# Optimization experiments

Measured on AMD Instinct MI355X. Metric: run time of the kernel, lower is better.

The kernel has to match this reference:

```python
import jax, jax.numpy as jnp
import numpy as np
from jax import lax

B, TIN, N, M, O, LM, TDEC = 64, 128, 256, 1024, 512, 2048, 64
LN_EPS = 1e-5


def setup_inputs() -> dict:
    key = jax.random.key(0)
    ks = jax.random.split(key, 32)
    s = 0.02
    p = lambda k, shape: (jax.random.normal(k, shape, jnp.float32) * s)
    z = lambda n: jnp.zeros((n,), jnp.float32)
    return {
        "X": jax.random.normal(ks[0], (B, TIN, N), jnp.float32),
        "Y0": jax.random.uniform(ks[1], (B, 1, O), jnp.float32),
        # encoder GRU, 2 layers (PyTorch layout: W_ih [3m,in], W_hh [3m,m])
        "enc_Wih0": p(ks[2], (3 * M, N)), "enc_Whh0": p(ks[3], (3 * M, M)),
        "enc_bih0": z(3 * M), "enc_bhh0": z(3 * M),
        "enc_Wih1": p(ks[4], (3 * M, M)), "enc_Whh1": p(ks[5], (3 * M, M)),
        "enc_bih1": z(3 * M), "enc_bhh1": z(3 * M),
        # decoder GRU, 2 layers (layer0 input dim = O)
        "dec_Wih0": p(ks[6], (3 * M, O)), "dec_Whh0": p(ks[7], (3 * M, M)),
        "dec_bih0": z(3 * M), "dec_bhh0": z(3 * M),
        "dec_Wih1": p(ks[8], (3 * M, M)), "dec_Whh1": p(ks[9], (3 * M, M)),
        "dec_bih1": z(3 * M), "dec_bhh1": z(3 * M),
        # decoder head
        "fc1_w": p(ks[10], (LM, M)), "fc1_b": z(LM),
        "ln_g": jnp.ones((LM,), jnp.float32), "ln_b": z(LM),
        "fc2_w": p(ks[11], (O, LM)), "fc2_b": z(O),
    }


def _gru_step(h, x, Wih, Whh, bih, bhh):
    # PyTorch GRU cell: gates ordered (r, z, n)
    gi = x @ Wih.T + bih          # [B, 3m]
    gh = h @ Whh.T + bhh          # [B, 3m]
    i_r, i_z, i_n = jnp.split(gi, 3, axis=-1)
    h_r, h_z, h_n = jnp.split(gh, 3, axis=-1)
    r = jax.nn.sigmoid(i_r + h_r)
    zg = jax.nn.sigmoid(i_z + h_z)
    n = jnp.tanh(i_n + r * h_n)
    return (1.0 - zg) * n + zg * h


def reference(X, Y0,
              enc_Wih0, enc_Whh0, enc_bih0, enc_bhh0,
              enc_Wih1, enc_Whh1, enc_bih1, enc_bhh1,
              dec_Wih0, dec_Whh0, dec_bih0, dec_bhh0,
              dec_Wih1, dec_Whh1, dec_bih1, dec_bhh1,
              fc1_w, fc1_b, ln_g, ln_b, fc2_w, fc2_b):
    batch = X.shape[0]
    # ---- encoder: 2-layer GRU over time ----
    seq = jnp.swapaxes(X, 0, 1)  # [T, B, n]
    enc_layers = [(enc_Wih0, enc_Whh0, enc_bih0, enc_bhh0),
                  (enc_Wih1, enc_Whh1, enc_bih1, enc_bhh1)]
    h_final = []
    for (Wih, Whh, bih, bhh) in enc_layers:
        def f(h, x, Wih=Wih, Whh=Whh, bih=bih, bhh=bhh):
            hn = _gru_step(h, x, Wih, Whh, bih, bhh)
            return hn, hn
        hT, seq = lax.scan(f, jnp.zeros((batch, M), X.dtype), seq)
        h_final.append(hT)

    dec0 = (dec_Wih0, dec_Whh0, dec_bih0, dec_bhh0)
    dec1 = (dec_Wih1, dec_Whh1, dec_bih1, dec_bhh1)
    y_init = Y0[:, 0, :]  # [B, o]

    def step(carry, _):
        h0, h1, y = carry
        h0n = _gru_step(h0, y, *dec0)
        h1n = _gru_step(h1, h0n, *dec1)
        z = h1n @ fc1_w.T + fc1_b                      # [B, l_m]
        mu = jnp.mean(z, axis=-1, keepdims=True)
        var = jnp.var(z, axis=-1, keepdims=True)
        z = (z - mu) * lax.rsqrt(var + LN_EPS) * ln_g + ln_b
        z = jax.nn.gelu(z, approximate=False)
        out = z @ fc2_w.T + fc2_b                      # [B, o]
        yn = jax.nn.softmax(out, axis=-1)
        return (h0n, h1n, yn), out

    _, outs = lax.scan(step, (h_final[0], h_final[1], y_init), None, length=TDEC)
    return jnp.swapaxes(outs, 0, 1)  # [B, TDEC, o]
```

## Files before the change

### kernel.cpp

```cpp
#include <hip/hip_runtime.h>
#include <math.h>

#define B 64
#define TIN 128
#define N_IN 256
#define M 1024
#define O_DIM 512
#define LM 2048
#define TDEC 64
#define M3 3072
#define CH 8

typedef short bf16x8 __attribute__((ext_vector_type(8)));
typedef float floatx4 __attribute__((ext_vector_type(4)));

__device__ __forceinline__ unsigned short f2bf(float f) {
    unsigned int u = __float_as_uint(f);
    u += 0x7FFFu + ((u >> 16) & 1u);
    return (unsigned short)(u >> 16);
}
__device__ __forceinline__ float sigm(float x) { return 1.f / (1.f + expf(-x)); }

__global__ __launch_bounds__(256) void cast_bf(const float* __restrict__ in,
                                               short* __restrict__ out, int n) {
    int i = blockIdx.x * 256 + threadIdx.x;
    if (i < n) out[i] = (short)f2bf(in[i]);
}

__global__ __launch_bounds__(256) void transpose_X_bf(const float* __restrict__ X,
                                                      short* __restrict__ Xt) {
    int idx = blockIdx.x * 256 + threadIdx.x;
    int n = idx & (N_IN - 1);
    int b = (idx >> 8) & (B - 1);
    int t = idx >> 14;
    Xt[idx] = (short)f2bf(X[(b * TIN + t) * N_IN + n]);
}

__global__ __launch_bounds__(256) void mfma_gemm_bias(
    const short* __restrict__ A, int lda,
    const short* __restrict__ W, int ldw,
    const float* __restrict__ bias,
    float* __restrict__ C, int ldc, int K) {
    int wave = threadIdx.x >> 6;
    int lane = threadIdx.x & 63;
    int r0 = blockIdx.y * 64 + wave * 16;
    int c0 = blockIdx.x * 16;
    int lrow = lane & 15;
    int ko8 = (lane >> 4) * 8;
    const short* ap = A + (size_t)(r0 + lrow) * lda + ko8;
    const short* wp = W + (size_t)(c0 + lrow) * ldw + ko8;
    floatx4 acc = {0.f, 0.f, 0.f, 0.f};
    #pragma unroll 4
    for (int k = 0; k < K; k += 32) {
        bf16x8 a = *(const bf16x8*)(ap + k);
        bf16x8 b = *(const bf16x8*)(wp + k);
        acc = __builtin_amdgcn_mfma_f32_16x16x32_bf16(a, b, acc, 0, 0, 0);
    }
    int col = c0 + lrow;
    float bv = bias[col];
    int rbase = r0 + (lane >> 4) * 4;
    #pragma unroll
    for (int i = 0; i < 4; i++)
        C[(size_t)(rbase + i) * ldc + col] = acc[i] + bv;
}

__global__ __launch_bounds__(256) void mfma_gemm_bias_ks(
    const short* __restrict__ A, int lda,
    const short* __restrict__ W, int ldw,
    const float* __restrict__ bias,
    float* __restrict__ C, int ldc, int K) {
    __shared__ float lds[4][64][4];
    int wave = threadIdx.x >> 6;
    int lane = threadIdx.x & 63;
    int r0 = blockIdx.y * 16;
    int c0 = blockIdx.x * 16;
    int Kq = K >> 2;
    int lrow = lane & 15;
    int ko8 = (lane >> 4) * 8;
    const short* ap = A + (size_t)(r0 + lrow) * lda + wave * Kq + ko8;
    const short* wp = W + (size_t)(c0 + lrow) * ldw + wave * Kq + ko8;
    floatx4 acc = {0.f, 0.f, 0.f, 0.f};
    #pragma unroll 4
    for (int k = 0; k < Kq; k += 32) {
        bf16x8 a = *(const bf16x8*)(ap + k);
        bf16x8 b = *(const bf16x8*)(wp + k);
        acc = __builtin_amdgcn_mfma_f32_16x16x32_bf16(a, b, acc, 0, 0, 0);
    }
    #pragma unroll
    for (int i = 0; i < 4; i++) lds[wave][lane][i] = acc[i];
    __syncthreads();
    int row = threadIdx.x >> 4, col = threadIdx.x & 15;
    int sl = (row >> 2) * 16 + col, rg = row & 3;
    float s = lds[0][sl][rg] + lds[1][sl][rg] + lds[2][sl][rg] + lds[3][sl][rg];
    C[(size_t)(r0 + row) * ldc + (c0 + col)] = s + bias[c0 + col];
}

__global__ __launch_bounds__(256) void gru_step_enc(
    const short* __restrict__ h_in_bf, const short* __restrict__ Whh,
    const float* __restrict__ gi, const float* __restrict__ bhh,
    float* __restrict__ h_f, short* __restrict__ h_out_bf,
    short* __restrict__ seq_out_bf) {
    __shared__ float lr[4][64][4], lz[4][64][4], lnn[4][64][4];
    int wave = threadIdx.x >> 6;
    int lane = threadIdx.x & 63;
    int m0 = blockIdx.x * 16;
    int r0 = blockIdx.y * 16;
    int lrow = lane & 15;
    int ko8 = (lane >> 4) * 8;
    const int Kq = M >> 2;
    const short* ap = h_in_bf + (size_t)(r0 + lrow) * M + wave * Kq + ko8;
    const short* wr = Whh + (size_t)(m0 + lrow) * M + wave * Kq + ko8;
    const short* wz = wr + (size_t)M * M;
    const short* wn = wr + (size_t)2 * M * M;
    floatx4 ar = {0.f, 0.f, 0.f, 0.f};
    floatx4 az = {0.f, 0.f, 0.f, 0.f};
    floatx4 ahn = {0.f, 0.f, 0.f, 0.f};
    #pragma unroll
    for (int k = 0; k < Kq; k += 32) {
        bf16x8 a = *(const bf16x8*)(ap + k);
        ar  = __builtin_amdgcn_mfma_f32_16x16x32_bf16(a, *(const bf16x8*)(wr + k), ar, 0, 0, 0);
        az  = __builtin_amdgcn_mfma_f32_16x16x32_bf16(a, *(const bf16x8*)(wz + k), az, 0, 0, 0);
        ahn = __builtin_amdgcn_mfma_f32_16x16x32_bf16(a, *(const bf16x8*)(wn + k), ahn, 0, 0, 0);
    }
    #pragma unroll
    for (int i = 0; i < 4; i++) {
        lr[wave][lane][i] = ar[i];
        lz[wave][lane][i] = az[i];
        lnn[wave][lane][i] = ahn[i];
    }
    __syncthreads();
    int row = threadIdx.x >> 4, col = threadIdx.x & 15;
    int sl = (row >> 2) * 16 + col, rg = row & 3;
    float sr = lr[0][sl][rg] + lr[1][sl][rg] + lr[2][sl][rg] + lr[3][sl][rg];
    float sz = lz[0][sl][rg] + lz[1][sl][rg] + lz[2][sl][rg] + lz[3][sl][rg];
    float sn = lnn[0][sl][rg] + lnn[1][sl][rg] + lnn[2][sl][rg] + lnn[3][sl][rg];
    int b = r0 + row, m = m0 + col;
    const float* gir = gi + (size_t)b * M3;
    float r = sigm(gir[m] + sr + bhh[m]);
    float z = sigm(gir[M + m] + sz + bhh[M + m]);
    float n = tanhf(gir[2 * M + m] + r * (sn + bhh[2 * M + m]));
    size_t hi = (size_t)b * M + m;
    float hv = (1.f - z) * n + z * h_f[hi];
    h_f[hi] = hv;
    short hb = (short)f2bf(hv);
    h_out_bf[hi] = hb;
    if (seq_out_bf) seq_out_bf[hi] = hb;
}

__global__ __launch_bounds__(256) void gru_step_dec(
    const short* __restrict__ x_bf, int Kx,
    const short* __restrict__ Wih,
    const short* __restrict__ h_in_bf, const short* __restrict__ Whh,
    const float* __restrict__ bih, const float* __restrict__ bhh,
    float* __restrict__ h_f, short* __restrict__ h_out_bf) {
    __shared__ float lr[4][64][4], lz[4][64][4], li[4][64][4], lh[4][64][4];
    int wave = threadIdx.x >> 6;
    int lane = threadIdx.x & 63;
    int m0 = blockIdx.x * 16;
    int r0 = blockIdx.y * 16;
    int lrow = lane & 15;
    int ko8 = (lane >> 4) * 8;
    floatx4 ar = {0.f, 0.f, 0.f, 0.f};
    floatx4 az = {0.f, 0.f, 0.f, 0.f};
    floatx4 ain = {0.f, 0.f, 0.f, 0.f};
    floatx4 ahn = {0.f, 0.f, 0.f, 0.f};
    {
        int Kq = Kx >> 2;
        const short* ap = x_bf + (size_t)(r0 + lrow) * Kx + wave * Kq + ko8;
        const short* wr = Wih + (size_t)(m0 + lrow) * Kx + wave * Kq + ko8;
        const short* wz = wr + (size_t)M * Kx;
        const short* wn = wr + (size_t)2 * M * Kx;
        #pragma unroll
        for (int k = 0; k < Kq; k += 32) {
            bf16x8 a = *(const bf16x8*)(ap + k);
            ar  = __builtin_amdgcn_mfma_f32_16x16x32_bf16(a, *(const bf16x8*)(wr + k), ar, 0, 0, 0);
            az  = __builtin_amdgcn_mfma_f32_16x16x32_bf16(a, *(const bf16x8*)(wz + k), az, 0, 0, 0);
            ain = __builtin_amdgcn_mfma_f32_16x16x32_bf16(a, *(const bf16x8*)(wn + k), ain, 0, 0, 0);
        }
    }
    {
        const int Kq = M >> 2;
        const short* ap = h_in_bf + (size_t)(r0 + lrow) * M + wave * Kq + ko8;
        const short* wr = Whh + (size_t)(m0 + lrow) * M + wave * Kq + ko8;
        const short* wz = wr + (size_t)M * M;
        const short* wn = wr + (size_t)2 * M * M;
        #pragma unroll
        for (int k = 0; k < Kq; k += 32) {
            bf16x8 a = *(const bf16x8*)(ap + k);
            ar  = __builtin_amdgcn_mfma_f32_16x16x32_bf16(a, *(const bf16x8*)(wr + k), ar, 0, 0, 0);
            az  = __builtin_amdgcn_mfma_f32_16x16x32_bf16(a, *(const bf16x8*)(wz + k), az, 0, 0, 0);
            ahn = __builtin_amdgcn_mfma_f32_16x16x32_bf16(a, *(const bf16x8*)(wn + k), ahn, 0, 0, 0);
        }
    }
    #pragma unroll
    for (int i = 0; i < 4; i++) {
        lr[wave][lane][i] = ar[i];
        lz[wave][lane][i] = az[i];
        li[wave][lane][i] = ain[i];
        lh[wave][lane][i] = ahn[i];
    }
    __syncthreads();
    int row = threadIdx.x >> 4, col = threadIdx.x & 15;
    int sl = (row >> 2) * 16 + col, rg = row & 3;
    float sr = lr[0][sl][rg] + lr[1][sl][rg] + lr[2][sl][rg] + lr[3][sl][rg];
    float sz = lz[0][sl][rg] + lz[1][sl][rg] + lz[2][sl][rg] + lz[3][sl][rg];
    float si = li[0][sl][rg] + li[1][sl][rg] + li[2][sl][rg] + li[3][sl][rg];
    float sh = lh[0][sl][rg] + lh[1][sl][rg] + lh[2][sl][rg] + lh[3][sl][rg];
    int b = r0 + row, m = m0 + col;
    float r = sigm(sr + bih[m] + bhh[m]);
    float z = sigm(sz + bih[M + m] + bhh[M + m]);
    float n = tanhf(si + bih[2 * M + m] + r * (sh + bhh[2 * M + m]));
    size_t hi = (size_t)b * M + m;
    float hv = (1.f - z) * n + z * h_f[hi];
    h_f[hi] = hv;
    h_out_bf[hi] = (short)f2bf(hv);
}

__global__ __launch_bounds__(256) void ln_gelu(const float* __restrict__ z,
                                               const float* __restrict__ g,
                                               const float* __restrict__ bt,
                                               short* __restrict__ zo) {
    __shared__ float red1[4], red2[4];
    int b = blockIdx.x, t = threadIdx.x;
    const float* row = z + (size_t)b * LM;
    float s = 0.f, ss = 0.f;
    for (int i = t; i < LM; i += 256) { float v = row[i]; s += v; ss += v * v; }
    #pragma unroll
    for (int off = 32; off > 0; off >>= 1) {
        s += __shfl_down(s, off, 64);
        ss += __shfl_down(ss, off, 64);
    }
    if ((t & 63) == 0) { red1[t >> 6] = s; red2[t >> 6] = ss; }
    __syncthreads();
    float S = red1[0] + red1[1] + red1[2] + red1[3];
    float SS = red2[0] + red2[1] + red2[2] + red2[3];
    float mu = S * (1.f / LM);
    float var = SS * (1.f / LM) - mu * mu;
    float inv = rsqrtf(var + 1e-5f);
    for (int i = t; i < LM; i += 256) {
        float v = (row[i] - mu) * inv * g[i] + bt[i];
        float gv = 0.5f * v * (1.f + erff(v * 0.70710678118654752f));
        zo[(size_t)b * LM + i] = (short)f2bf(gv);
    }
}

__global__ __launch_bounds__(256) void softmax_row(const float* __restrict__ logits,
                                                   int ldl, short* __restrict__ y) {
    __shared__ float redm[4], reds[4];
    int b = blockIdx.x, t = threadIdx.x;
    const float* row = logits + (size_t)b * ldl;
    float v0 = row[t], v1 = row[t + 256];
    float mx = fmaxf(v0, v1);
    #pragma unroll
    for (int off = 32; off > 0; off >>= 1) mx = fmaxf(mx, __shfl_down(mx, off, 64));
    if ((t & 63) == 0) redm[t >> 6] = mx;
    __syncthreads();
    mx = fmaxf(fmaxf(redm[0], redm[1]), fmaxf(redm[2], redm[3]));
    float e0 = expf(v0 - mx), e1 = expf(v1 - mx);
    float s = e0 + e1;
    #pragma unroll
    for (int off = 32; off > 0; off >>= 1) s += __shfl_down(s, off, 64);
    if ((t & 63) == 0) reds[t >> 6] = s;
    __syncthreads();
    s = reds[0] + reds[1] + reds[2] + reds[3];
    float inv = 1.f / s;
    y[b * O_DIM + t] = (short)f2bf(e0 * inv);
    y[b * O_DIM + t + 256] = (short)f2bf(e1 * inv);
}

extern "C" void kernel_launch(void* const* d_in, const int* in_sizes, int n_in,
                              void* d_out, int out_size, void* d_ws, size_t ws_size,
                              hipStream_t stream) {
    const float* X        = (const float*)d_in[0];
    const float* Y0       = (const float*)d_in[1];
    const float* enc_Wih0 = (const float*)d_in[2];
    const float* enc_Whh0 = (const float*)d_in[3];
    const float* enc_bih0 = (const float*)d_in[4];
    const float* enc_bhh0 = (const float*)d_in[5];
    const float* enc_Wih1 = (const float*)d_in[6];
    const float* enc_Whh1 = (const float*)d_in[7];
    const float* enc_bih1 = (const float*)d_in[8];
    const float* enc_bhh1 = (const float*)d_in[9];
    const float* dec_Wih0 = (const float*)d_in[10];
    const float* dec_Whh0 = (const float*)d_in[11];
    const float* dec_bih0 = (const float*)d_in[12];
    const float* dec_bhh0 = (const float*)d_in[13];
    const float* dec_Wih1 = (const float*)d_in[14];
    const float* dec_Whh1 = (const float*)d_in[15];
    const float* dec_bih1 = (const float*)d_in[16];
    const float* dec_bhh1 = (const float*)d_in[17];
    const float* fc1_w    = (const float*)d_in[18];
    const float* fc1_b    = (const float*)d_in[19];
    const float* ln_g     = (const float*)d_in[20];
    const float* ln_b     = (const float*)d_in[21];
    const float* fc2_w    = (const float*)d_in[22];
    const float* fc2_b    = (const float*)d_in[23];
    float* out = (float*)d_out;

    char* p = (char*)d_ws;
    auto carve = [&](size_t bytes) {
        void* r = p;
        p += (bytes + 255) & ~(size_t)255;
        return r;
    };
    short* Xt    = (short*)carve((size_t)TIN * B * N_IN * 2);
    short* seqA  = (short*)carve((size_t)TIN * B * M * 2);
    float* gi_ch = (float*)carve((size_t)CH * B * M3 * 4);
    short* we_ih0 = (short*)carve((size_t)M3 * N_IN * 2);
    short* we_hh0 = (short*)carve((size_t)M3 * M * 2);
    short* we_ih1 = (short*)carve((size_t)M3 * M * 2);
    short* we_hh1 = (short*)carve((size_t)M3 * M * 2);
    short* wd_ih0 = (short*)carve((size_t)M3 * O_DIM * 2);
    short* wd_hh0 = (short*)carve((size_t)M3 * M * 2);
    short* wd_ih1 = (short*)carve((size_t)M3 * M * 2);
    short* wd_hh1 = (short*)carve((size_t)M3 * M * 2);
    short* wfc1   = (short*)carve((size_t)LM * M * 2);
    short* wfc2   = (short*)carve((size_t)O_DIM * LM * 2);
    float* h0f = (float*)carve((size_t)B * M * 4);
    float* h1f = (float*)carve((size_t)B * M * 4);
    short* h0b = (short*)carve((size_t)2 * B * M * 2);
    short* h1b = (short*)carve((size_t)2 * B * M * 2);
    short* yb  = (short*)carve((size_t)B * O_DIM * 2);
    float* zb  = (float*)carve((size_t)B * LM * 4);
    short* zbb = (short*)carve((size_t)B * LM * 2);

    auto cast = [&](const float* src, short* dst, int n) {
        cast_bf<<<(n + 255) / 256, 256, 0, stream>>>(src, dst, n);
    };
    cast(enc_Wih0, we_ih0, M3 * N_IN);
    cast(enc_Whh0, we_hh0, M3 * M);
    cast(enc_Wih1, we_ih1, M3 * M);
    cast(enc_Whh1, we_hh1, M3 * M);
    cast(dec_Wih0, wd_ih0, M3 * O_DIM);
    cast(dec_Whh0, wd_hh0, M3 * M);
    cast(dec_Wih1, wd_ih1, M3 * M);
    cast(dec_Whh1, wd_hh1, M3 * M);
    cast(fc1_w, wfc1, LM * M);
    cast(fc2_w, wfc2, O_DIM * LM);
    cast(Y0, yb, B * O_DIM);
    transpose_X_bf<<<(TIN * B * N_IN) / 256, 256, 0, stream>>>(X, Xt);

    hipMemsetAsync(h0f, 0, (size_t)B * M * 4, stream);
    hipMemsetAsync(h1f, 0, (size_t)B * M * 4, stream);
    hipMemsetAsync(h0b, 0, (size_t)B * M * 2, stream);
    hipMemsetAsync(h1b, 0, (size_t)B * M * 2, stream);

    dim3 gruGrid(M / 16, B / 16);

    for (int layer = 0; layer < 2; layer++) {
        const short* Wih = layer ? we_ih1 : we_ih0;
        const short* Whh = layer ? we_hh1 : we_hh0;
        const float* bih = layer ? enc_bih1 : enc_bih0;
        const float* bhh = layer ? enc_bhh1 : enc_bhh0;
        const short* inseq = layer ? seqA : Xt;
        const int Kin = layer ? M : N_IN;
        float* hf = layer ? h1f : h0f;
        short* hb = layer ? h1b : h0b;
        for (int c = 0; c < TIN / CH; c++) {
            mfma_gemm_bias<<<dim3(M3 / 16, CH * B / 64), 256, 0, stream>>>(
                inseq + (size_t)c * CH * B * Kin, Kin, Wih, Kin, bih,
                gi_ch, M3, Kin);
            for (int tt = 0; tt < CH; tt++) {
                int t = c * CH + tt;
                int pin = t & 1, pout = pin ^ 1;
                short* so = (layer == 0) ? (seqA + (size_t)t * B * M) : nullptr;
                gru_step_enc<<<gruGrid, 256, 0, stream>>>(
                    hb + (size_t)pin * B * M, Whh,
                    gi_ch + (size_t)tt * B * M3, bhh,
                    hf, hb + (size_t)pout * B * M, so);
            }
        }
    }

    for (int t = 0; t < TDEC; t++) {
        int pin = t & 1, pout = pin ^ 1;
        gru_step_dec<<<gruGrid, 256, 0, stream>>>(
            yb, O_DIM, wd_ih0,
            h0b + (size_t)pin * B * M, wd_hh0,
            dec_bih0, dec_bhh0, h0f, h0b + (size_t)pout * B * M);
        gru_step_dec<<<gruGrid, 256, 0, stream>>>(
            h0b + (size_t)pout * B * M, M, wd_ih1,
            h1b + (size_t)pin * B * M, wd_hh1,
            dec_bih1, dec_bhh1, h1f, h1b + (size_t)pout * B * M);
        mfma_gemm_bias_ks<<<dim3(LM / 16, B / 16), 256, 0, stream>>>(
            h1b + (size_t)pout * B * M, M, wfc1, M, fc1_b, zb, LM, M);
        ln_gelu<<<B, 256, 0, stream>>>(zb, ln_g, ln_b, zbb);
        mfma_gemm_bias_ks<<<dim3(O_DIM / 16, B / 16), 256, 0, stream>>>(
            zbb, LM, wfc2, LM, fc2_b, out + (size_t)t * O_DIM, TDEC * O_DIM, LM);
        softmax_row<<<B, 256, 0, stream>>>(out + (size_t)t * O_DIM,
                                           TDEC * O_DIM, yb);
    }
}
```

Before: 5.534 ms.

## Replace per-step kernel launches with persistent encoder/decoder megakernels using grid barriers

Collapses the hundreds of per-timestep kernel launches for the encoder GRU and the decoder loop into two persistent kernels of 128 blocks that synchronise through a software grid barrier built on atomics. Each block now handles two output column tiles per step. Softmax is fused into the next decoder step's input staging in LDS, and LayerNorm statistics are accumulated through a stats buffer. The aim is to remove launch overhead and inter-kernel gaps on a latency-bound recurrence. In exchange, all blocks must be co-resident for the barrier to work, the barrier spin adds latency, and the barrier has a timeout guard that could break synchronisation silently.

```diff
diff --git a/kernel.cpp b/kernel.cpp
--- a/kernel.cpp
+++ b/kernel.cpp
@@ -10,6 +10,7 @@
 #define TDEC 64
 #define M3 3072
 #define CH 8
+#define NB 128
 
 typedef short bf16x8 __attribute__((ext_vector_type(8)));
 typedef float floatx4 __attribute__((ext_vector_type(4)));
@@ -20,6 +21,27 @@
     return (unsigned short)(u >> 16);
 }
 __device__ __forceinline__ float sigm(float x) { return 1.f / (1.f + expf(-x)); }
+
+__device__ __forceinline__ void gridbar(unsigned* cnt, unsigned* eps, unsigned epoch) {
+    __syncthreads();
+    if (threadIdx.x == 0) {
+        unsigned old = __hip_atomic_fetch_add(cnt, 1u, __ATOMIC_ACQ_REL,
+                                              __HIP_MEMORY_SCOPE_AGENT);
+        if (old == NB - 1) {
+            __hip_atomic_store(cnt, 0u, __ATOMIC_RELAXED, __HIP_MEMORY_SCOPE_AGENT);
+            __hip_atomic_store(eps, epoch, __ATOMIC_RELEASE, __HIP_MEMORY_SCOPE_AGENT);
+        } else {
+            unsigned guard = 0;
+            while (__hip_atomic_load(eps, __ATOMIC_RELAXED,
+                                     __HIP_MEMORY_SCOPE_AGENT) < epoch) {
+                __builtin_amdgcn_s_sleep(2);
+                if (++guard > (1u << 24)) break;
+            }
+            __builtin_amdgcn_fence(__ATOMIC_ACQUIRE, "agent");
+        }
+    }
+    __syncthreads();
+}
 
 __global__ __launch_bounds__(256) void cast_bf(const float* __restrict__ in,
                                                short* __restrict__ out, int n) {
@@ -36,236 +58,432 @@
     Xt[idx] = (short)f2bf(X[(b * TIN + t) * N_IN + n]);
 }
 
-__global__ __launch_bounds__(256) void mfma_gemm_bias(
-    const short* __restrict__ A, int lda,
-    const short* __restrict__ W, int ldw,
-    const float* __restrict__ bias,
-    float* __restrict__ C, int ldc, int K) {
-    int wave = threadIdx.x >> 6;
-    int lane = threadIdx.x & 63;
-    int r0 = blockIdx.y * 64 + wave * 16;
-    int c0 = blockIdx.x * 16;
-    int lrow = lane & 15;
-    int ko8 = (lane >> 4) * 8;
-    const short* ap = A + (size_t)(r0 + lrow) * lda + ko8;
-    const short* wp = W + (size_t)(c0 + lrow) * ldw + ko8;
-    floatx4 acc = {0.f, 0.f, 0.f, 0.f};
-    #pragma unroll 4
-    for (int k = 0; k < K; k += 32) {
-        bf16x8 a = *(const bf16x8*)(ap + k);
-        bf16x8 b = *(const bf16x8*)(wp + k);
-        acc = __builtin_amdgcn_mfma_f32_16x16x32_bf16(a, b, acc, 0, 0, 0);
+struct EncArgs {
+    const short* Xt;
+    short* seqA;
+    float* gi;
+    const short* wih0; const short* whh0; const float* bih0; const float* bhh0;
+    const short* wih1; const short* whh1; const float* bih1; const float* bhh1;
+    float* h0f; float* h1f;
+    short* h0b; short* h1b;
+    unsigned* cnt; unsigned* eps;
+};
+
+__global__ __launch_bounds__(256, 1) void enc_mega(EncArgs a) {
+    __shared__ float lds[2][3][4][64][4];
+    const int bid  = blockIdx.x;
+    const int wave = threadIdx.x >> 6;
+    const int lane = threadIdx.x & 63;
+    const int lrow = lane & 15;
+    const int ko8  = (lane >> 4) * 8;
+    unsigned epoch = 0;
+
+    for (int layer = 0; layer < 2; ++layer) {
+        const short* Wih = layer ? a.wih1 : a.wih0;
+        const short* Whh = layer ? a.whh1 : a.whh0;
+        const float* bih = layer ? a.bih1 : a.bih0;
+        const float* bhh = layer ? a.bhh1 : a.bhh0;
+        const short* inseq = layer ? a.seqA : a.Xt;
+        const int K = layer ? M : N_IN;
+        float* hf = layer ? a.h1f : a.h0f;
+        short* hb = layer ? a.h1b : a.h0b;
+
+        for (int c = 0; c < TIN / CH; ++c) {
+            {
+                const short* A = inseq + (size_t)c * CH * B * K;
+                int gw = bid * 4 + wave;
+                for (int i = 0; i < 12; ++i) {
+                    int tile = gw * 12 + i;
+                    int r0 = (tile / 192) * 16;
+                    int c0 = (tile % 192) * 16;
+                    const short* ap = A + (size_t)(r0 + lrow) * K + ko8;
+                    const short* wp = Wih + (size_t)(c0 + lrow) * K + ko8;
+                    floatx4 acc = {0.f, 0.f, 0.f, 0.f};
+                    #pragma unroll 4
+                    for (int k = 0; k < K; k += 32) {
+                        bf16x8 av = *(const bf16x8*)(ap + k);
+                        bf16x8 bv = *(const bf16x8*)(wp + k);
+                        acc = __builtin_amdgcn_mfma_f32_16x16x32_bf16(av, bv, acc, 0, 0, 0);
+                    }
+                    int col = c0 + lrow;
+                    float bv = bih[col];
+                    int rb = r0 + (lane >> 4) * 4;
+                    #pragma unroll
+                    for (int q = 0; q < 4; q++)
+                        a.gi[(size_t)(rb + q) * M3 + col] = acc[q] + bv;
+                }
+            }
+            gridbar(a.cnt, a.eps, ++epoch);
+            for (int tt = 0; tt < CH; ++tt) {
+                int t = c * CH + tt;
+                int pin = t & 1, pout = pin ^ 1;
+                const short* h_in = hb + (size_t)pin * B * M;
+                const float* gi_t = a.gi + (size_t)tt * B * M3;
+                int r0 = (bid & 3) * 16;
+                const int Kq = M >> 2;
+                const short* ap0 = h_in + (size_t)(r0 + lrow) * M + wave * Kq + ko8;
+                const short *wr[2], *wz[2], *wn[2];
+                #pragma unroll
+                for (int j = 0; j < 2; ++j) {
+                    int m0 = (j * 32 + (bid >> 2)) * 16;
+                    wr[j] = Whh + (size_t)(m0 + lrow) * M + wave * Kq + ko8;
+                    wz[j] = wr[j] + (size_t)M * M;
+                    wn[j] = wr[j] + (size_t)2 * M * M;
+                }
+                floatx4 ar[2], az[2], ah[2];
+                #pragma unroll
+                for (int j = 0; j < 2; ++j) {
+                    ar[j] = (floatx4){0.f, 0.f, 0.f, 0.f};
+                    az[j] = (floatx4){0.f, 0.f, 0.f, 0.f};
+                    ah[j] = (floatx4){0.f, 0.f, 0.f, 0.f};
+                }
+                #pragma unroll
+                for (int k = 0; k < Kq; k += 32) {
+                    bf16x8 av = *(const bf16x8*)(ap0 + k);
+                    #pragma unroll
+                    for (int j = 0; j < 2; ++j) {
+                        ar[j] = __builtin_amdgcn_mfma_f32_16x16x32_bf16(av, *(const bf16x8*)(wr[j] + k), ar[j], 0, 0, 0);
+                        az[j] = __builtin_amdgcn_mfma_f32_16x16x32_bf16(av, *(const bf16x8*)(wz[j] + k), az[j], 0, 0, 0);
+                        ah[j] = __builtin_amdgcn_mfma_f32_16x16x32_bf16(av, *(const bf16x8*)(wn[j] + k), ah[j], 0, 0, 0);
+                    }
+                }
+                #pragma unroll
+                for (int j = 0; j < 2; ++j)
+                    #pragma unroll
+                    for (int i = 0; i < 4; i++) {
+                        lds[j][0][wave][lane][i] = ar[j][i];
+                        lds[j][1][wave][lane][i] = az[j][i];
+                        lds[j][2][wave][lane][i] = ah[j][i];
+                    }
+                __syncthreads();
+                int row = threadIdx.x >> 4, col = threadIdx.x & 15;
+                int sl = (row >> 2) * 16 + col, rg = row & 3;
+                int b = r0 + row;
+                const float* gir = gi_t + (size_t)b * M3;
+                #pragma unroll
+                for (int j = 0; j < 2; ++j) {
+                    int m0 = (j * 32 + (bid >> 2)) * 16;
+                    int m = m0 + col;
+                    float sr = lds[j][0][0][sl][rg] + lds[j][0][1][sl][rg] + lds[j][0][2][sl][rg] + lds[j][0][3][sl][rg];
+                    float sz = lds[j][1][0][sl][rg] + lds[j][1][1][sl][rg] + lds[j][1][2][sl][rg] + lds[j][1][3][sl][rg];
+                    float sn = lds[j][2][0][sl][rg] + lds[j][2][1][sl][rg] + lds[j][2][2][sl][rg] + lds[j][2][3][sl][rg];
+                    float r = sigm(gir[m] + sr + bhh[m]);
+                    float z = sigm(gir[M + m] + sz + bhh[M + m]);
+                    float n = tanhf(gir[2 * M + m] + r * (sn + bhh[2 * M + m]));
+                    size_t hi = (size_t)b * M + m;
+                    float hv = (1.f - z) * n + z * hf[hi];
+                    hf[hi] = hv;
+                    short hbv = (short)f2bf(hv);
+                    hb[(size_t)pout * B * M + hi] = hbv;
+                    if (layer == 0) a.seqA[(size_t)t * B * M + hi] = hbv;
+                }
+                gridbar(a.cnt, a.eps, ++epoch);
+            }
+        }
     }
-    int col = c0 + lrow;
-    float bv = bias[col];
-    int rbase = r0 + (lane >> 4) * 4;
-    #pragma unroll
-    for (int i = 0; i < 4; i++)
-        C[(size_t)(rbase + i) * ldc + col] = acc[i] + bv;
-}
-
-__global__ __launch_bounds__(256) void mfma_gemm_bias_ks(
-    const short* __restrict__ A, int lda,
-    const short* __restrict__ W, int ldw,
-    const float* __restrict__ bias,
-    float* __restrict__ C, int ldc, int K) {
-    __shared__ float lds[4][64][4];
-    int wave = threadIdx.x >> 6;
-    int lane = threadIdx.x & 63;
-    int r0 = blockIdx.y * 16;
-    int c0 = blockIdx.x * 16;
-    int Kq = K >> 2;
-    int lrow = lane & 15;
-    int ko8 = (lane >> 4) * 8;
-    const short* ap = A + (size_t)(r0 + lrow) * lda + wave * Kq + ko8;
-    const short* wp = W + (size_t)(c0 + lrow) * ldw + wave * Kq + ko8;
-    floatx4 acc = {0.f, 0.f, 0.f, 0.f};
-    #pragma unroll 4
-    for (int k = 0; k < Kq; k += 32) {
-        bf16x8 a = *(const bf16x8*)(ap + k);
-        bf16x8 b = *(const bf16x8*)(wp + k);
-        acc = __builtin_amdgcn_mfma_f32_16x16x32_bf16(a, b, acc, 0, 0, 0);
+}
+
+struct DecArgs {
+    const short* yb;
+    const short* wih0; const short* whh0; const float* bih0; const float* bhh0;
+    const short* wih1; const short* whh1; const float* bih1; const float* bhh1;
+    const short* wfc1; const float* fc1b;
+    const float* lng; const float* lnb;
+    const short* wfc2; const float* fc2b;
+    float* h0f; float* h1f;
+    short* h0b; short* h1b;
+    float* zb;
+    short* zbb;
+    float* stats;
+    float* out;
+    unsigned* cnt; unsigned* eps;
+};
+
+__global__ __launch_bounds__(256, 1) void dec_mega(DecArgs a) {
+    __shared__ short xs[16 * O_DIM];
+    __shared__ float lds[2][4][4][64][4];
+    const int bid  = blockIdx.x;
+    const int wave = threadIdx.x >> 6;
+    const int lane = threadIdx.x & 63;
+    const int lrow = lane & 15;
+    const int ko8  = (lane >> 4) * 8;
+    const int ldl  = TDEC * O_DIM;
+    unsigned epoch = 0;
+
+    for (int t = 0; t < TDEC; ++t) {
+        int pin = t & 1, pout = pin ^ 1;
+        int r0 = (bid & 3) * 16;
+        {
+            int rr = wave * 4 + (lane >> 4);
+            int cl = lane & 15;
+            if (t > 0) {
+                const float* rowp = a.out + (size_t)(r0 + rr) * ldl
+                                  + (size_t)(t - 1) * O_DIM + cl * 32;
+                float v[32];
+                float mx = -3.4e38f;
+                #pragma unroll
+                for (int j = 0; j < 32; j++) { v[j] = rowp[j]; mx = fmaxf(mx, v[j]); }
+                #pragma unroll
+                for (int off = 1; off < 16; off <<= 1) mx = fmaxf(mx, __shfl_xor(mx, off, 16));
+                float s = 0.f;
+                #pragma unroll
+                for (int j = 0; j < 32; j++) { v[j] = __expf(v[j] - mx); s += v[j]; }
+                #pragma unroll
+                for (int off = 1; off < 16; off <<= 1) s += __shfl_xor(s, off, 16);
+                float inv = 1.f / s;
+                #pragma unroll
+                for (int j = 0; j < 32; j += 2) {
+                    unsigned int pk = (unsigned int)f2bf(v[j] * inv)
+                                    | ((unsigned int)f2bf(v[j + 1] * inv) << 16);
+                    int byte = ((rr * O_DIM + cl * 32 + j) * 2) ^ ((rr & 7) << 4);
+                    *(unsigned int*)((char*)xs + byte) = pk;
+                }
+            } else {
+                const short* rowp = a.yb + (size_t)(r0 + rr) * O_DIM + cl * 32;
+                #pragma unroll
+                for (int j = 0; j < 32; j += 2) {
+                    unsigned int pk = (unsigned int)(unsigned short)rowp[j]
+                                    | ((unsigned int)(unsigned short)rowp[j + 1] << 16);
+                    int byte = ((rr * O_DIM + cl * 32 + j) * 2) ^ ((rr & 7) << 4);
+                    *(unsigned int*)((char*)xs + byte) = pk;
+                }
+            }
+            __syncthreads();
+            const int KqI = O_DIM >> 2;
+            const int KqH = M >> 2;
+            const short *wrI[2], *wzI[2], *wnI[2], *wrH[2], *wzH[2], *wnH[2];
+            #pragma unroll
+            for (int j = 0; j < 2; ++j) {
+                int m0 = (j * 32 + (bid >> 2)) * 16;
+                wrI[j] = a.wih0 + (size_t)(m0 + lrow) * O_DIM + wave * KqI + ko8;
+                wzI[j] = wrI[j] + (size_t)M * O_DIM;
+                wnI[j] = wrI[j] + (size_t)2 * M * O_DIM;
+                wrH[j] = a.whh0 + (size_t)(m0 + lrow) * M + wave * KqH + ko8;
+                wzH[j] = wrH[j] + (size_t)M * M;
+                wnH[j] = wrH[j] + (size_t)2 * M * M;
+            }
+            floatx4 ar[2], az[2], ai[2], ah[2];
+            #pragma unroll
+            for (int j = 0; j < 2; ++j) {
+                ar[j] = (floatx4){0.f, 0.f, 0.f, 0.f};
+                az[j] = (floatx4){0.f, 0.f, 0.f, 0.f};
+                ai[j] = (floatx4){0.f, 0.f, 0.f, 0.f};
+                ah[j] = (floatx4){0.f, 0.f, 0.f, 0.f};
+            }
+            #pragma unroll
+            for (int k = 0; k < KqI; k += 32) {
+                int abyte = ((lrow * O_DIM + wave * KqI + ko8 + k) * 2) ^ ((lrow & 7) << 4);
+                bf16x8 av = *(const bf16x8*)((const char*)xs + abyte);
+                #pragma unroll
+                for (int j = 0; j < 2; ++j) {
+                    ar[j] = __builtin_amdgcn_mfma_f32_16x16x32_bf16(av, *(const bf16x8*)(wrI[j] + k), ar[j], 0, 0, 0);
+                    az[j] = __builtin_amdgcn_mfma_f32_16x16x32_bf16(av, *(const bf16x8*)(wzI[j] + k), az[j], 0, 0, 0);
+                    ai[j] = __builtin_amdgcn_mfma_f32_16x16x32_bf16(av, *(const bf16x8*)(wnI[j] + k), ai[j], 0, 0, 0);
+                }
+            }
+            const short* apH = a.h0b + (size_t)pin * B * M + (size_t)(r0 + lrow) * M + wave * KqH + ko8;
+            #pragma unroll
+            for (int k = 0; k < KqH; k += 32) {
+                bf16x8 av = *(const bf16x8*)(apH + k);
+                #pragma unroll
+                for (int j = 0; j < 2; ++j) {
+                    ar[j] = __builtin_amdgcn_mfma_f32_16x16x32_bf16(av, *(const bf16x8*)(wrH[j] + k), ar[j], 0, 0, 0);
+                    az[j] = __builtin_amdgcn_mfma_f32_16x16x32_bf16(av, *(const bf16x8*)(wzH[j] + k), az[j], 0, 0, 0);
+                    ah[j] = __builtin_amdgcn_mfma_f32_16x16x32_bf16(av, *(const bf16x8*)(wnH[j] + k), ah[j], 0, 0, 0);
+                }
+            }
+            #pragma unroll
+            for (int j = 0; j < 2; ++j)
+                #pragma unroll
+                for (int i = 0; i < 4; i++) {
+                    lds[j][0][wave][lane][i] = ar[j][i];
+                    lds[j][1][wave][lane][i] = az[j][i];
+                    lds[j][2][wave][lane][i] = ai[j][i];
+                    lds[j][3][wave][lane][i] = ah[j][i];
+                }
+            __syncthreads();
+            int row = threadIdx.x >> 4, col = threadIdx.x & 15;
+            int sl = (row >> 2) * 16 + col, rg = row & 3;
+            int b = r0 + row;
+            #pragma unroll
+            for (int j = 0; j < 2; ++j) {
+                int m0 = (j * 32 + (bid >> 2)) * 16;
+                int m = m0 + col;
+                float sr = lds[j][0][0][sl][rg] + lds[j][0][1][sl][rg] + lds[j][0][2][sl][rg] + lds[j][0][3][sl][rg];
+                float sz = lds[j][1][0][sl][rg] + lds[j][1][1][sl][rg] + lds[j][1][2][sl][rg] + lds[j][1][3][sl][rg];
+                float si = lds[j][2][0][sl][rg] + lds[j][2][1][sl][rg] + lds[j][2][2][sl][rg] + lds[j][2][3][sl][rg];
+                float sh = lds[j][3][0][sl][rg] + lds[j][3][1][sl][rg] + lds[j][3][2][sl][rg] + lds[j][3][3][sl][rg];
+                float r = sigm(sr + a.bih0[m] + a.bhh0[m]);
+                float z = sigm(sz + a.bih0[M + m] + a.bhh0[M + m]);
+                float n = tanhf(si + a.bih0[2 * M + m] + r * (sh + a.bhh0[2 * M + m]));
+                size_t hi = (size_t)b * M + m;
+                float hv = (1.f - z) * n + z * a.h0f[hi];
+                a.h0f[hi] = hv;
+                a.h0b[(size_t)pout * B * M + hi] = (short)f2bf(hv);
+            }
+        }
+        gridbar(a.cnt, a.eps, ++epoch);
+        {
+            const int Kq = M >> 2;
+            const short *wrI[2], *wzI[2], *wnI[2], *wrH[2], *wzH[2], *wnH[2];
+            #pragma unroll
+            for (int j = 0; j < 2; ++j) {
+                int m0 = (j * 32 + (bid >> 2)) * 16;
+                wrI[j] = a.wih1 + (size_t)(m0 + lrow) * M + wave * Kq + ko8;
+                wzI[j] = wrI[j] + (size_t)M * M;
+                wnI[j] = wrI[j] + (size_t)2 * M * M;
+                wrH[j] = a.whh1 + (size_t)(m0 + lrow) * M + wave * Kq + ko8;
+                wzH[j] = wrH[j] + (size_t)M * M;
+                wnH[j] = wrH[j] + (size_t)2 * M * M;
+            }
+            floatx4 ar[2], az[2], ai[2], ah[2];
+            #pragma unroll
+            for (int j = 0; j < 2; ++j) {
+                ar[j] = (floatx4){0.f, 0.f, 0.f, 0.f};
+                az[j] = (floatx4){0.f, 0.f, 0.f, 0.f};
+                ai[j] = (floatx4){0.f, 0.f, 0.f, 0.f};
+                ah[j] = (floatx4){0.f, 0.f, 0.f, 0.f};
+            }
+            const short* apI = a.h0b + (size_t)pout * B * M + (size_t)(r0 + lrow) * M + wave * Kq + ko8;
+            #pragma unroll
+            for (int k = 0; k < Kq; k += 32) {
+                bf16x8 av = *(const bf16x8*)(apI + k);
+                #pragma unroll
+                for (int j = 0; j < 2; ++j) {
+                    ar[j] = __builtin_amdgcn_mfma_f32_16x16x32_bf16(av, *(const bf16x8*)(wrI[j] + k), ar[j], 0, 0, 0);
+                    az[j] = __builtin_amdgcn_mfma_f32_16x16x32_bf16(av, *(const bf16x8*)(wzI[j] + k), az[j], 0, 0, 0);
+                    ai[j] = __builtin_amdgcn_mfma_f32_16x16x32_bf16(av, *(const bf16x8*)(wnI[j] + k), ai[j], 0, 0, 0);
+                }
+            }
+            const short* apH = a.h1b + (size_t)pin * B * M + (size_t)(r0 + lrow) * M + wave * Kq + ko8;
+            #pragma unroll
+            for (int k = 0; k < Kq; k += 32) {
+                bf16x8 av = *(const bf16x8*)(apH + k);
+                #pragma unroll
+                for (int j = 0; j < 2; ++j) {
+                    ar[j] = __builtin_amdgcn_mfma_f32_16x16x32_bf16(av, *(const bf16x8*)(wrH[j] + k), ar[j], 0, 0, 0);
+                    az[j] = __builtin_amdgcn_mfma_f32_16x16x32_bf16(av, *(const bf16x8*)(wzH[j] + k), az[j], 0, 0, 0);
+                    ah[j] = __builtin_amdgcn_mfma_f32_16x16x32_bf16(av, *(const bf16x8*)(wnH[j] + k), ah[j], 0, 0, 0);
+                }
+            }
+            #pragma unroll
+            for (int j = 0; j < 2; ++j)
+                #pragma unroll
+                for (int i = 0; i < 4; i++) {
+                    lds[j][0][wave][lane][i] = ar[j][i];
+                    lds[j][1][wave][lane][i] = az[j][i];
+                    lds[j][2][wave][lane][i] = ai[j][i];
+                    lds[j][3][wave][lane][i] = ah[j][i];
+                }
+            __syncthreads();
+            int row = threadIdx.x >> 4, col = threadIdx.x & 15;
+            int sl = (row >> 2) * 16 + col, rg = row & 3;
+            int b = r0 + row;
+            #pragma unroll
+            for (int j = 0; j < 2; ++j) {
+                int m0 = (j * 32 + (bid >> 2)) * 16;
+                int m = m0 + col;
+                float sr = lds[j][0][0][sl][rg] + lds[j][0][1][sl][rg] + lds[j][0][2][sl][rg] + lds[j][0][3][sl][rg];
+                float sz = lds[j][1][0][sl][rg] + lds[j][1][1][sl][rg] + lds[j][1][2][sl][rg] + lds[j][1][3][sl][rg];
+                float si = lds[j][2][0][sl][rg] + lds[j][2][1][sl][rg] + lds[j][2][2][sl][rg] + lds[j][2][3][sl][rg];
+                float sh = lds[j][3][0][sl][rg] + lds[j][3][1][sl][rg] + lds[j][3][2][sl][rg] + lds[j][3][3][sl][rg];
+                float r = sigm(sr + a.bih1[m] + a.bhh1[m]);
+                float z = sigm(sz + a.bih1[M + m] + a.bhh1[M + m]);
+                float n = tanhf(si + a.bih1[2 * M + m] + r * (sh + a.bhh1[2 * M + m]));
+                size_t hi = (size_t)b * M + m;
+                float hv = (1.f - z) * n + z * a.h1f[hi];
+                a.h1f[hi] = hv;
+                a.h1b[(size_t)pout * B * M + hi] = (short)f2bf(hv);
+            }
+        }
+        gridbar(a.cnt, a.eps, ++epoch);
+        {
+            float* st = a.stats + (size_t)t * 2 * B;
+            const int Kq = M >> 2;
+            const short* ap = a.h1b + (size_t)pout * B * M + (size_t)(r0 + lrow) * M + wave * Kq + ko8;
+            const short* wp[4];
+            floatx4 acc[4];
+            #pragma unroll
+            for (int j = 0; j < 4; ++j) {
+                int c0 = (j * 32 + (bid >> 2)) * 16;
+                wp[j] = a.wfc1 + (size_t)(c0 + lrow) * M + wave * Kq + ko8;
+                acc[j] = (floatx4){0.f, 0.f, 0.f, 0.f};
+            }
+            #pragma unroll
+            for (int k = 0; k < Kq; k += 32) {
+                bf16x8 av = *(const bf16x8*)(ap + k);
+                #pragma unroll
+                for (int j = 0; j < 4; ++j)
+                    acc[j] = __builtin_amdgcn_mfma_f32_16x16x32_bf16(av, *(const bf16x8*)(wp[j] + k), acc[j], 0, 0, 0);
+            }
+            #pragma unroll
+            for (int j = 0; j < 4; ++j)
+                #pragma unroll
+                for (int i = 0; i < 4; i++) lds[0][j][wave][lane][i] = acc[j][i];
+            __syncthreads();
+            int row = threadIdx.x >> 4, col = threadIdx.x & 15;
+            int sl = (row >> 2) * 16 + col, rg = row & 3;
+            #pragma unroll
+            for (int j = 0; j < 4; ++j) {
+                int c0 = (j * 32 + (bid >> 2)) * 16;
+                float s = lds[0][j][0][sl][rg] + lds[0][j][1][sl][rg]
+                        + lds[0][j][2][sl][rg] + lds[0][j][3][sl][rg];
+                float val = s + a.fc1b[c0 + col];
+                a.zb[(size_t)(r0 + row) * LM + c0 + col] = val;
+                float sv = val, sq = val * val;
+                #pragma unroll
+                for (int off = 1; off < 16; off <<= 1) {
+                    sv += __shfl_xor(sv, off, 16);
+                    sq += __shfl_xor(sq, off, 16);
+                }
+                if ((threadIdx.x & 15) == 0) {
+                    atomicAdd(&st[r0 + row], sv);
+                    atomicAdd(&st[B + r0 + row], sq);
+                }
+            }
+        }
+        gridbar(a.cnt, a.eps, ++epoch);
+        {
+            const float* st = a.stats + (size_t)t * 2 * B;
+            int e0 = (bid * 256 + threadIdx.x) * 4;
+            int rowd = e0 >> 11;
+            float mu = st[rowd] * (1.f / LM);
+            float var = st[B + rowd] * (1.f / LM) - mu * mu;
+            float inv = rsqrtf(var + 1e-5f);
+            #pragma unroll
+            for (int j = 0; j < 4; j++) {
+                int e = e0 + j;
+                int cc = e & (LM - 1);
+                float zn = (a.zb[e] - mu) * inv * a.lng[cc] + a.lnb[cc];
+                float ge = 0.5f * zn * (1.f + erff(zn * 0.70710678118654752f));
+                a.zbb[e] = (short)f2bf(ge);
+            }
+        }
+        gridbar(a.cnt, a.eps, ++epoch);
+        {
+            int c0 = (bid >> 2) * 16;
+            const int Kq = LM >> 2;
+            const short* ap = a.zbb + (size_t)(r0 + lrow) * LM + wave * Kq + ko8;
+            const short* wpp = a.wfc2 + (size_t)(c0 + lrow) * LM + wave * Kq + ko8;
+            floatx4 acc = {0.f, 0.f, 0.f, 0.f};
+            #pragma unroll 4
+            for (int k = 0; k < Kq; k += 32) {
+                bf16x8 av = *(const bf16x8*)(ap + k);
+                bf16x8 bv = *(const bf16x8*)(wpp + k);
+                acc = __builtin_amdgcn_mfma_f32_16x16x32_bf16(av, bv, acc, 0, 0, 0);
+            }
+            #pragma unroll
+            for (int i = 0; i < 4; i++) lds[0][0][wave][lane][i] = acc[i];
+            __syncthreads();
+            int row = threadIdx.x >> 4, col = threadIdx.x & 15;
+            int sl = (row >> 2) * 16 + col, rg = row & 3;
+            float s = lds[0][0][0][sl][rg] + lds[0][0][1][sl][rg]
+                    + lds[0][0][2][sl][rg] + lds[0][0][3][sl][rg];
+            a.out[(size_t)(r0 + row) * ldl + (size_t)t * O_DIM + c0 + col]
+                = s + a.fc2b[c0 + col];
+        }
+        gridbar(a.cnt, a.eps, ++epoch);
     }
-    #pragma unroll
-    for (int i = 0; i < 4; i++) lds[wave][lane][i] = acc[i];
-    __syncthreads();
-    int row = threadIdx.x >> 4, col = threadIdx.x & 15;
-    int sl = (row >> 2) * 16 + col, rg = row & 3;
-    float s = lds[0][sl][rg] + lds[1][sl][rg] + lds[2][sl][rg] + lds[3][sl][rg];
-    C[(size_t)(r0 + row) * ldc + (c0 + col)] = s + bias[c0 + col];
-}
-
-__global__ __launch_bounds__(256) void gru_step_enc(
-    const short* __restrict__ h_in_bf, const short* __restrict__ Whh,
-    const float* __restrict__ gi, const float* __restrict__ bhh,
-    float* __restrict__ h_f, short* __restrict__ h_out_bf,
-    short* __restrict__ seq_out_bf) {
-    __shared__ float lr[4][64][4], lz[4][64][4], lnn[4][64][4];
-    int wave = threadIdx.x >> 6;
-    int lane = threadIdx.x & 63;
-    int m0 = blockIdx.x * 16;
-    int r0 = blockIdx.y * 16;
-    int lrow = lane & 15;
-    int ko8 = (lane >> 4) * 8;
-    const int Kq = M >> 2;
-    const short* ap = h_in_bf + (size_t)(r0 + lrow) * M + wave * Kq + ko8;
-    const short* wr = Whh + (size_t)(m0 + lrow) * M + wave * Kq + ko8;
-    const short* wz = wr + (size_t)M * M;
-    const short* wn = wr + (size_t)2 * M * M;
-    floatx4 ar = {0.f, 0.f, 0.f, 0.f};
-    floatx4 az = {0.f, 0.f, 0.f, 0.f};
-    floatx4 ahn = {0.f, 0.f, 0.f, 0.f};
-    #pragma unroll
-    for (int k = 0; k < Kq; k += 32) {
-        bf16x8 a = *(const bf16x8*)(ap + k);
-        ar  = __builtin_amdgcn_mfma_f32_16x16x32_bf16(a, *(const bf16x8*)(wr + k), ar, 0, 0, 0);
-        az  = __builtin_amdgcn_mfma_f32_16x16x32_bf16(a, *(const bf16x8*)(wz + k), az, 0, 0, 0);
-        ahn = __builtin_amdgcn_mfma_f32_16x16x32_bf16(a, *(const bf16x8*)(wn + k), ahn, 0, 0, 0);
-    }
-    #pragma unroll
-    for (int i = 0; i < 4; i++) {
-        lr[wave][lane][i] = ar[i];
-        lz[wave][lane][i] = az[i];
-        lnn[wave][lane][i] = ahn[i];
-    }
-    __syncthreads();
-    int row = threadIdx.x >> 4, col = threadIdx.x & 15;
-    int sl = (row >> 2) * 16 + col, rg = row & 3;
-    float sr = lr[0][sl][rg] + lr[1][sl][rg] + lr[2][sl][rg] + lr[3][sl][rg];
-    float sz = lz[0][sl][rg] + lz[1][sl][rg] + lz[2][sl][rg] + lz[3][sl][rg];
-    float sn = lnn[0][sl][rg] + lnn[1][sl][rg] + lnn[2][sl][rg] + lnn[3][sl][rg];
-    int b = r0 + row, m = m0 + col;
-    const float* gir = gi + (size_t)b * M3;
-    float r = sigm(gir[m] + sr + bhh[m]);
-    float z = sigm(gir[M + m] + sz + bhh[M + m]);
-    float n = tanhf(gir[2 * M + m] + r * (sn + bhh[2 * M + m]));
-    size_t hi = (size_t)b * M + m;
-    float hv = (1.f - z) * n + z * h_f[hi];
-    h_f[hi] = hv;
-    short hb = (short)f2bf(hv);
-    h_out_bf[hi] = hb;
-    if (seq_out_bf) seq_out_bf[hi] = hb;
-}
-
-__global__ __launch_bounds__(256) void gru_step_dec(
-    const short* __restrict__ x_bf, int Kx,
-    const short* __restrict__ Wih,
-    const short* __restrict__ h_in_bf, const short* __restrict__ Whh,
-    const float* __restrict__ bih, const float* __restrict__ bhh,
-    float* __restrict__ h_f, short* __restrict__ h_out_bf) {
-    __shared__ float lr[4][64][4], lz[4][64][4], li[4][64][4], lh[4][64][4];
-    int wave = threadIdx.x >> 6;
-    int lane = threadIdx.x & 63;
-    int m0 = blockIdx.x * 16;
-    int r0 = blockIdx.y * 16;
-    int lrow = lane & 15;
-    int ko8 = (lane >> 4) * 8;
-    floatx4 ar = {0.f, 0.f, 0.f, 0.f};
-    floatx4 az = {0.f, 0.f, 0.f, 0.f};
-    floatx4 ain = {0.f, 0.f, 0.f, 0.f};
-    floatx4 ahn = {0.f, 0.f, 0.f, 0.f};
-    {
-        int Kq = Kx >> 2;
-        const short* ap = x_bf + (size_t)(r0 + lrow) * Kx + wave * Kq + ko8;
-        const short* wr = Wih + (size_t)(m0 + lrow) * Kx + wave * Kq + ko8;
-        const short* wz = wr + (size_t)M * Kx;
-        const short* wn = wr + (size_t)2 * M * Kx;
-        #pragma unroll
-        for (int k = 0; k < Kq; k += 32) {
-            bf16x8 a = *(const bf16x8*)(ap + k);
-            ar  = __builtin_amdgcn_mfma_f32_16x16x32_bf16(a, *(const bf16x8*)(wr + k), ar, 0, 0, 0);
-            az  = __builtin_amdgcn_mfma_f32_16x16x32_bf16(a, *(const bf16x8*)(wz + k), az, 0, 0, 0);
-            ain = __builtin_amdgcn_mfma_f32_16x16x32_bf16(a, *(const bf16x8*)(wn + k), ain, 0, 0, 0);
-        }
-    }
-    {
-        const int Kq = M >> 2;
-        const short* ap = h_in_bf + (size_t)(r0 + lrow) * M + wave * Kq + ko8;
-        const short* wr = Whh + (size_t)(m0 + lrow) * M + wave * Kq + ko8;
-        const short* wz = wr + (size_t)M * M;
-        const short* wn = wr + (size_t)2 * M * M;
-        #pragma unroll
-        for (int k = 0; k < Kq; k += 32) {
-            bf16x8 a = *(const bf16x8*)(ap + k);
-            ar  = __builtin_amdgcn_mfma_f32_16x16x32_bf16(a, *(const bf16x8*)(wr + k), ar, 0, 0, 0);
-            az  = __builtin_amdgcn_mfma_f32_16x16x32_bf16(a, *(const bf16x8*)(wz + k), az, 0, 0, 0);
-            ahn = __builtin_amdgcn_mfma_f32_16x16x32_bf16(a, *(const bf16x8*)(wn + k), ahn, 0, 0, 0);
-        }
-    }
-    #pragma unroll
-    for (int i = 0; i < 4; i++) {
-        lr[wave][lane][i] = ar[i];
-        lz[wave][lane][i] = az[i];
-        li[wave][lane][i] = ain[i];
-        lh[wave][lane][i] = ahn[i];
-    }
-    __syncthreads();
-    int row = threadIdx.x >> 4, col = threadIdx.x & 15;
-    int sl = (row >> 2) * 16 + col, rg = row & 3;
-    float sr = lr[0][sl][rg] + lr[1][sl][rg] + lr[2][sl][rg] + lr[3][sl][rg];
-    float sz = lz[0][sl][rg] + lz[1][sl][rg] + lz[2][sl][rg] + lz[3][sl][rg];
-    float si = li[0][sl][rg] + li[1][sl][rg] + li[2][sl][rg] + li[3][sl][rg];
-    float sh = lh[0][sl][rg] + lh[1][sl][rg] + lh[2][sl][rg] + lh[3][sl][rg];
-    int b = r0 + row, m = m0 + col;
-    float r = sigm(sr + bih[m] + bhh[m]);
-    float z = sigm(sz + bih[M + m] + bhh[M + m]);
-    float n = tanhf(si + bih[2 * M + m] + r * (sh + bhh[2 * M + m]));
-    size_t hi = (size_t)b * M + m;
-    float hv = (1.f - z) * n + z * h_f[hi];
-    h_f[hi] = hv;
-    h_out_bf[hi] = (short)f2bf(hv);
-}
-
-__global__ __launch_bounds__(256) void ln_gelu(const float* __restrict__ z,
-                                               const float* __restrict__ g,
-                                               const float* __restrict__ bt,
-                                               short* __restrict__ zo) {
-    __shared__ float red1[4], red2[4];
-    int b = blockIdx.x, t = threadIdx.x;
-    const float* row = z + (size_t)b * LM;
-    float s = 0.f, ss = 0.f;
-    for (int i = t; i < LM; i += 256) { float v = row[i]; s += v; ss += v * v; }
-    #pragma unroll
-    for (int off = 32; off > 0; off >>= 1) {
-        s += __shfl_down(s, off, 64);
-        ss += __shfl_down(ss, off, 64);
-    }
-    if ((t & 63) == 0) { red1[t >> 6] = s; red2[t >> 6] = ss; }
-    __syncthreads();
-    float S = red1[0] + red1[1] + red1[2] + red1[3];
-    float SS = red2[0] + red2[1] + red2[2] + red2[3];
-    float mu = S * (1.f / LM);
-    float var = SS * (1.f / LM) - mu * mu;
-    float inv = rsqrtf(var + 1e-5f);
-    for (int i = t; i < LM; i += 256) {
-        float v = (row[i] - mu) * inv * g[i] + bt[i];
-        float gv = 0.5f * v * (1.f + erff(v * 0.70710678118654752f));
-        zo[(size_t)b * LM + i] = (short)f2bf(gv);
-    }
-}
-
-__global__ __launch_bounds__(256) void softmax_row(const float* __restrict__ logits,
-                                                   int ldl, short* __restrict__ y) {
-    __shared__ float redm[4], reds[4];
-    int b = blockIdx.x, t = threadIdx.x;
-    const float* row = logits + (size_t)b * ldl;
-    float v0 = row[t], v1 = row[t + 256];
-    float mx = fmaxf(v0, v1);
-    #pragma unroll
-    for (int off = 32; off > 0; off >>= 1) mx = fmaxf(mx, __shfl_down(mx, off, 64));
-    if ((t & 63) == 0) redm[t >> 6] = mx;
-    __syncthreads();
-    mx = fmaxf(fmaxf(redm[0], redm[1]), fmaxf(redm[2], redm[3]));
-    float e0 = expf(v0 - mx), e1 = expf(v1 - mx);
-    float s = e0 + e1;
-    #pragma unroll
-    for (int off = 32; off > 0; off >>= 1) s += __shfl_down(s, off, 64);
-    if ((t & 63) == 0) reds[t >> 6] = s;
-    __syncthreads();
-    s = reds[0] + reds[1] + reds[2] + reds[3];
-    float inv = 1.f / s;
-    y[b * O_DIM + t] = (short)f2bf(e0 * inv);
-    y[b * O_DIM + t + 256] = (short)f2bf(e1 * inv);
 }
 
 extern "C" void kernel_launch(void* const* d_in, const int* in_sizes, int n_in,
@@ -323,6 +541,9 @@
     short* yb  = (short*)carve((size_t)B * O_DIM * 2);
     float* zb  = (float*)carve((size_t)B * LM * 4);
     short* zbb = (short*)carve((size_t)B * LM * 2);
+    float* lnstats = (float*)carve((size_t)TDEC * 2 * B * 4);
+    unsigned* ebar = (unsigned*)carve(256);
+    unsigned* dbar = (unsigned*)carve(256);
 
     auto cast = [&](const float* src, short* dst, int n) {
         cast_bf<<<(n + 255) / 256, 256, 0, stream>>>(src, dst, n);
@@ -344,50 +565,27 @@
     hipMemsetAsync(h1f, 0, (size_t)B * M * 4, stream);
     hipMemsetAsync(h0b, 0, (size_t)B * M * 2, stream);
     hipMemsetAsync(h1b, 0, (size_t)B * M * 2, stream);
-
-    dim3 gruGrid(M / 16, B / 16);
-
-    for (int layer = 0; layer < 2; layer++) {
-        const short* Wih = layer ? we_ih1 : we_ih0;
-        const short* Whh = layer ? we_hh1 : we_hh0;
-        const float* bih = layer ? enc_bih1 : enc_bih0;
-        const float* bhh = layer ? enc_bhh1 : enc_bhh0;
-        const short* inseq = layer ? seqA : Xt;
-        const int Kin = layer ? M : N_IN;
-        float* hf = layer ? h1f : h0f;
-        short* hb = layer ? h1b : h0b;
-        for (int c = 0; c < TIN / CH; c++) {
-            mfma_gemm_bias<<<dim3(M3 / 16, CH * B / 64), 256, 0, stream>>>(
-                inseq + (size_t)c * CH * B * Kin, Kin, Wih, Kin, bih,
-                gi_ch, M3, Kin);
-            for (int tt = 0; tt < CH; tt++) {
-                int t = c * CH + tt;
-                int pin = t & 1, pout = pin ^ 1;
-                short* so = (layer == 0) ? (seqA + (size_t)t * B * M) : nullptr;
-                gru_step_enc<<<gruGrid, 256, 0, stream>>>(
-                    hb + (size_t)pin * B * M, Whh,
-                    gi_ch + (size_t)tt * B * M3, bhh,
-                    hf, hb + (size_t)pout * B * M, so);
-            }
-        }
-    }
-
-    for (int t = 0; t < TDEC; t++) {
-        int pin = t & 1, pout = pin ^ 1;
-        gru_step_dec<<<gruGrid, 256, 0, stream>>>(
-            yb, O_DIM, wd_ih0,
-            h0b + (size_t)pin * B * M, wd_hh0,
-            dec_bih0, dec_bhh0, h0f, h0b + (size_t)pout * B * M);
-        gru_step_dec<<<gruGrid, 256, 0, stream>>>(
-            h0b + (size_t)pout * B * M, M, wd_ih1,
-            h1b + (size_t)pin * B * M, wd_hh1,
-            dec_bih1, dec_bhh1, h1f, h1b + (size_t)pout * B * M);
-        mfma_gemm_bias_ks<<<dim3(LM / 16, B / 16), 256, 0, stream>>>(
-            h1b + (size_t)pout * B * M, M, wfc1, M, fc1_b, zb, LM, M);
-        ln_gelu<<<B, 256, 0, stream>>>(zb, ln_g, ln_b, zbb);
-        mfma_gemm_bias_ks<<<dim3(O_DIM / 16, B / 16), 256, 0, stream>>>(
-            zbb, LM, wfc2, LM, fc2_b, out + (size_t)t * O_DIM, TDEC * O_DIM, LM);
-        softmax_row<<<B, 256, 0, stream>>>(out + (size_t)t * O_DIM,
-                                           TDEC * O_DIM, yb);
-    }
-}
+    hipMemsetAsync(lnstats, 0, (size_t)TDEC * 2 * B * 4, stream);
+    hipMemsetAsync(ebar, 0, 256, stream);
+    hipMemsetAsync(dbar, 0, 256, stream);
+
+    EncArgs ea;
+    ea.Xt = Xt; ea.seqA = seqA; ea.gi = gi_ch;
+    ea.wih0 = we_ih0; ea.whh0 = we_hh0; ea.bih0 = enc_bih0; ea.bhh0 = enc_bhh0;
+    ea.wih1 = we_ih1; ea.whh1 = we_hh1; ea.bih1 = enc_bih1; ea.bhh1 = enc_bhh1;
+    ea.h0f = h0f; ea.h1f = h1f; ea.h0b = h0b; ea.h1b = h1b;
+    ea.cnt = ebar; ea.eps = ebar + 16;
+    enc_mega<<<dim3(NB), dim3(256), 0, stream>>>(ea);
+
+    DecArgs da;
+    da.yb = yb;
+    da.wih0 = wd_ih0; da.whh0 = wd_hh0; da.bih0 = dec_bih0; da.bhh0 = dec_bhh0;
+    da.wih1 = wd_ih1; da.whh1 = wd_hh1; da.bih1 = dec_bih1; da.bhh1 = dec_bhh1;
+    da.wfc1 = wfc1; da.fc1b = fc1_b;
+    da.lng = ln_g; da.lnb = ln_b;
+    da.wfc2 = wfc2; da.fc2b = fc2_b;
+    da.h0f = h0f; da.h1f = h1f; da.h0b = h0b; da.h1b = h1b;
+    da.zb = zb; da.zbb = zbb; da.stats = lnstats; da.out = out;
+    da.cnt = dbar; da.eps = dbar + 16;
+    dec_mega<<<dim3(NB), dim3(256), 0, stream>>>(da);
+}
```

After: 14.55 ms. 163% more time.
